# Optimization experiments

Measured on AMD Instinct MI355X. Metric: run time of the kernel, lower is better.

Reference implementation:

```python
import jax, jax.numpy as jnp
import numpy as np

B, I, H = 16384, 512, 512


def _linear_params(key, out_dim, in_dim):
    kw, kb = jax.random.split(key)
    bound = 1.0 / np.sqrt(in_dim)
    W = jax.random.uniform(kw, (out_dim, in_dim), jnp.float32, -bound, bound)
    b = jax.random.uniform(kb, (out_dim,), jnp.float32, -bound, bound)
    return W, b


def setup_inputs() -> dict:
    key = jax.random.key(0)
    ks = jax.random.split(key, 12)
    x = jax.random.normal(ks[0], (B, I), jnp.float32)
    h_prev = jax.random.normal(ks[1], (B, H), jnp.float32)
    c_prev = jax.random.normal(ks[2], (B, H), jnp.float32)
    W_xi, b_xi = _linear_params(ks[3], H, I)
    W_hi, b_hi = _linear_params(ks[4], H, H)
    W_xf, b_xf = _linear_params(ks[5], H, I)
    W_hf, b_hf = _linear_params(ks[6], H, H)
    W_xc, b_xc = _linear_params(ks[7], H, I)
    W_hc, b_hc = _linear_params(ks[8], H, H)
    W_xo, b_xo = _linear_params(ks[9], H, I)
    W_ho, b_ho = _linear_params(ks[10], H, H)
    W_e, b_e = _linear_params(ks[11], H, I + H)
    return dict(x=x, h_prev=h_prev, c_prev=c_prev,
                W_xi=W_xi, b_xi=b_xi, W_hi=W_hi, b_hi=b_hi,
                W_xf=W_xf, b_xf=b_xf, W_hf=W_hf, b_hf=b_hf,
                W_xc=W_xc, b_xc=b_xc, W_hc=W_hc, b_hc=b_hc,
                W_xo=W_xo, b_xo=b_xo, W_ho=W_ho, b_ho=b_ho,
                W_e=W_e, b_e=b_e)


def reference(x, h_prev, c_prev,
              W_xi, b_xi, W_hi, b_hi,
              W_xf, b_xf, W_hf, b_hf,
              W_xc, b_xc, W_hc, b_hc,
              W_xo, b_xo, W_ho, b_ho,
              W_e, b_e):
    # Batch the 4 input-to-hidden projections into one GEMM and the 4
    # hidden-to-hidden projections into another (same math as 8 Linears).
    Wx = jnp.concatenate([W_xi, W_xf, W_xc, W_xo], axis=0)   # [4H, I]
    bx = jnp.concatenate([b_xi, b_xf, b_xc, b_xo], axis=0)   # [4H]
    Wh = jnp.concatenate([W_hi, W_hf, W_hc, W_ho], axis=0)   # [4H, H]
    bh = jnp.concatenate([b_hi, b_hf, b_hc, b_ho], axis=0)
    gates = (x @ Wx.T + bx) + (h_prev @ Wh.T + bh)            # [B, 4H]
    gi, gf, gc, go = jnp.split(gates, 4, axis=-1)
    i = jax.nn.sigmoid(gi)
    f = jax.nn.sigmoid(gf)
    g = jnp.tanh(gc)
    o = jax.nn.sigmoid(go)
    c = f * c_prev + i * g
    # exp gate: Linear on [x, h_prev] -> tanh -> exp; split W_e to avoid concat
    We_x, We_h = W_e[:, :x.shape[-1]], W_e[:, x.shape[-1]:]
    exp_factor = jnp.exp(jnp.tanh(x @ We_x.T + h_prev @ We_h.T + b_e))
    h = o * jnp.tanh(c) * exp_factor
    return (h, c)
```

## Files before the change

### kernel.cpp

```cpp
#include <hip/hip_runtime.h>
#include <stdint.h>

#define Bsz 16384
#define Hh  512
#define Kd  1024
#define BM  256
#define BNJ 32
#define BK  64
#define NT  16

typedef __attribute__((ext_vector_type(8))) short bf16x8;
typedef __attribute__((ext_vector_type(4))) float f32x4;
typedef __attribute__((ext_vector_type(8))) unsigned short u16x8;

__device__ __forceinline__ unsigned short f2bf(float f) {
    union { float f; unsigned u; } v; v.f = f;
    unsigned u = v.u;
    return (unsigned short)((u + 0x7fffu + ((u >> 16) & 1u)) >> 16);
}
__device__ __forceinline__ float fast_tanh(float x) {
    float e = __expf(2.f * x);
    return (e - 1.f) / (e + 1.f);
}
__device__ __forceinline__ float fast_sigmoid(float x) {
    return 1.f / (1.f + __expf(-x));
}

__global__ void pack_A(const float* __restrict__ x, const float* __restrict__ h,
                       unsigned short* __restrict__ A) {
    const long total = (long)Bsz * Kd / 8;
    for (long i = (long)blockIdx.x * blockDim.x + threadIdx.x; i < total;
         i += (long)gridDim.x * blockDim.x) {
        long row = i >> 7;
        int  col = ((int)(i & 127)) << 3;
        const float* src = (col < 512) ? (x + row * 512 + col)
                                       : (h + row * 512 + (col - 512));
        float4 f0 = *(const float4*)(src);
        float4 f1 = *(const float4*)(src + 4);
        u16x8 o;
        o[0]=f2bf(f0.x); o[1]=f2bf(f0.y); o[2]=f2bf(f0.z); o[3]=f2bf(f0.w);
        o[4]=f2bf(f1.x); o[5]=f2bf(f1.y); o[6]=f2bf(f1.z); o[7]=f2bf(f1.w);
        *(u16x8*)(A + (i << 3)) = o;
    }
}

__global__ void pack_B(const float* __restrict__ Wxi, const float* __restrict__ Whi,
                       const float* __restrict__ Wxf, const float* __restrict__ Whf,
                       const float* __restrict__ Wxc, const float* __restrict__ Whc,
                       const float* __restrict__ Wxo, const float* __restrict__ Who,
                       const float* __restrict__ We,
                       const float* __restrict__ bxi, const float* __restrict__ bhi,
                       const float* __restrict__ bxf, const float* __restrict__ bhf,
                       const float* __restrict__ bxc, const float* __restrict__ bhc,
                       const float* __restrict__ bxo, const float* __restrict__ bho,
                       const float* __restrict__ be,
                       unsigned short* __restrict__ Bp, float* __restrict__ bias) {
    const long id = (long)blockIdx.x * blockDim.x + threadIdx.x;
    if (id < 327680) {
        int blk = (int)(id >> 6);
        int l   = (int)(id & 63);
        int kh  = blk & 1;
        int kt  = (blk >> 1) & 15;
        int rest = blk >> 5;
        int g    = rest % 5;
        int jgrp = rest / 5;
        int j  = jgrp * 16 + (l & 15);
        int k0 = kt * 64 + kh * 32 + ((l >> 4) << 3);
        const float* src;
        if (g == 4) {
            src = We + (long)j * 1024 + k0;
        } else {
            const float* Wx = (g == 0) ? Wxi : (g == 1) ? Wxf : (g == 2) ? Wxc : Wxo;
            const float* Wh = (g == 0) ? Whi : (g == 1) ? Whf : (g == 2) ? Whc : Who;
            src = (k0 < 512) ? (Wx + (long)j * 512 + k0)
                             : (Wh + (long)j * 512 + (k0 - 512));
        }
        float4 f0 = *(const float4*)(src);
        float4 f1 = *(const float4*)(src + 4);
        u16x8 o;
        o[0]=f2bf(f0.x); o[1]=f2bf(f0.y); o[2]=f2bf(f0.z); o[3]=f2bf(f0.w);
        o[4]=f2bf(f1.x); o[5]=f2bf(f1.y); o[6]=f2bf(f1.z); o[7]=f2bf(f1.w);
        *(u16x8*)(Bp + (long)blk * 512 + l * 8) = o;
    }
    if (id < 2560) {
        int row = (int)id;
        int g = row >> 9, j = row & 511;
        float b;
        if (g == 4) b = be[j];
        else {
            const float* bx = (g == 0) ? bxi : (g == 1) ? bxf : (g == 2) ? bxc : bxo;
            const float* bh = (g == 0) ? bhi : (g == 1) ? bhf : (g == 2) ? bhc : bho;
            b = bx[j] + bh[j];
        }
        bias[row] = b;
    }
}

#define GL16(g, l) __builtin_amdgcn_global_load_lds( \
    (const __attribute__((address_space(1))) unsigned int*)(g), \
    (__attribute__((address_space(3))) unsigned int*)(l), 16, 0, 0)

#define WAITVM(n) asm volatile("s_waitcnt vmcnt(" #n ")" ::: "memory")
#define WAITLGKM0() asm volatile("s_waitcnt lgkmcnt(0)" ::: "memory")
#define BARRIER() asm volatile("s_barrier" ::: "memory")

#define STAGE_A(BUF, T) do { \
    _Pragma("unroll") \
    for (int it_ = 0; it_ < 4; ++it_) { \
        int c_   = it_ * 512 + tid; \
        int row_ = c_ >> 3; \
        int ch_  = c_ & 7; \
        const unsigned short* src_ = A + (brow + row_) * (long)Kd + (T) * BK \
                                     + ((ch_ ^ (row_ & 7)) << 3); \
        GL16(src_, &Alds[BUF][c_ << 3]); \
    } \
} while (0)

#define LOADB(BN, T) do { \
    const unsigned short* bsrc_ = Bp + ((long)(jgrp * 160) + (T) * 2) * 512 + lane * 8; \
    _Pragma("unroll") \
    for (int g_ = 0; g_ < 5; ++g_) { \
        _Pragma("unroll") \
        for (int kh_ = 0; kh_ < 2; ++kh_) { \
            asm volatile("global_load_dwordx4 %0, %1, off" \
                : "=v"(BN[g_ * 2 + kh_]) \
                : "v"(bsrc_ + (g_ * 32 + kh_) * 512)); \
        } \
    } \
} while (0)

#define LOADA_FRAGS(BUF) do { \
    _Pragma("unroll") \
    for (int m_ = 0; m_ < 4; ++m_) { \
        int r_ = wm * 64 + m_ * 16 + fr; \
        _Pragma("unroll") \
        for (int kh_ = 0; kh_ < 2; ++kh_) { \
            af[m_][kh_] = *(const bf16x8*)&Alds[BUF][r_ * 64 + \
                ((((kh_ << 2) | q) ^ (fr & 7)) << 3)]; \
        } \
    } \
} while (0)

#define MFMA_CLUSTER(BC) do { \
    __builtin_amdgcn_s_setprio(1); \
    _Pragma("unroll") \
    for (int g_ = 0; g_ < 5; ++g_) \
        _Pragma("unroll") \
        for (int m_ = 0; m_ < 4; ++m_) \
            _Pragma("unroll") \
            for (int kh_ = 0; kh_ < 2; ++kh_) \
                acc[g_][m_] = __builtin_amdgcn_mfma_f32_16x16x32_bf16( \
                    af[m_][kh_], BC[g_ * 2 + kh_], acc[g_][m_], 0, 0, 0); \
    __builtin_amdgcn_s_setprio(0); \
} while (0)

#define ITER(T, BUF, BCUR, BNXT, WA, WB, IA, IB) do { \
    WAITVM(WA); \
    BARRIER(); \
    LOADA_FRAGS(BUF); \
    WAITLGKM0(); \
    BARRIER(); \
    if (IB) LOADB(BNXT, (T) + 1); \
    if (IA) STAGE_A(BUF, (T) + 2); \
    WAITVM(WB); \
    __builtin_amdgcn_sched_barrier(0); \
    MFMA_CLUSTER(BCUR); \
} while (0)

__global__ __launch_bounds__(512, 2)
void xlstm_gemm(const unsigned short* __restrict__ A,
                const unsigned short* __restrict__ Bp,
                const float* __restrict__ bias,
                const float* __restrict__ c_prev,
                float* __restrict__ out) {
    __shared__ __align__(16) unsigned short Alds[2][BM * BK];

    const int tid  = threadIdx.x;
    const int wid  = tid >> 6;
    const int lane = tid & 63;
    const int wm   = wid >> 1;
    const int wj   = wid & 1;
    const int fr   = lane & 15;
    const int q    = lane >> 4;

    const int orig = blockIdx.x;
    const int wg   = (orig & 7) * 128 + (orig >> 3);
    const int mblk = wg >> 4;
    const int jblk = wg & 15;
    const long brow = (long)mblk * BM;
    const int  bcol = jblk * BNJ;
    const int  jgrp = jblk * 2 + wj;

    f32x4 acc[5][4];
#pragma unroll
    for (int g = 0; g < 5; ++g)
#pragma unroll
        for (int m = 0; m < 4; ++m)
#pragma unroll
            for (int r = 0; r < 4; ++r) acc[g][m][r] = 0.f;

    bf16x8 af[4][2];
    bf16x8 BA[10], BB[10];

    STAGE_A(0, 0);
    LOADB(BA, 0);
    STAGE_A(1, 1);

    for (int t = 0; t < 14; t += 2) {
        ITER(t,     0, BA, BB, 14, 18, 1, 1);
        ITER(t + 1, 1, BB, BA, 14, 18, 1, 1);
    }
    ITER(14, 0, BA, BB, 14, 14, 0, 1);
    ITER(15, 1, BB, BA, 10,  0, 0, 0);

    const int j = bcol + wj * 16 + fr;
    const float bi_ = bias[j];
    const float bf_ = bias[512 + j];
    const float bc_ = bias[1024 + j];
    const float bo_ = bias[1536 + j];
    const float be_ = bias[2048 + j];
    const long mbase = brow + wm * 64 + (q << 2);
#pragma unroll
    for (int m = 0; m < 4; ++m) {
#pragma unroll
        for (int r = 0; r < 4; ++r) {
            long row = mbase + m * 16 + r;
            float gi = acc[0][m][r] + bi_;
            float gf = acc[1][m][r] + bf_;
            float gc = acc[2][m][r] + bc_;
            float go = acc[3][m][r] + bo_;
            float ge = acc[4][m][r] + be_;
            float iv = fast_sigmoid(gi);
            float fv = fast_sigmoid(gf);
            float gv = fast_tanh(gc);
            float ov = fast_sigmoid(go);
            float ef = __expf(fast_tanh(ge));
            float cp = c_prev[row * 512 + j];
            float cv = fv * cp + iv * gv;
            float hv = ov * fast_tanh(cv) * ef;
            out[row * 512 + j] = hv;
            out[(long)Bsz * 512 + row * 512 + j] = cv;
        }
    }
}

extern "C" void kernel_launch(void* const* d_in, const int* in_sizes, int n_in,
                              void* d_out, int out_size, void* d_ws, size_t ws_size,
                              hipStream_t stream) {
    const float* x      = (const float*)d_in[0];
    const float* h_prev = (const float*)d_in[1];
    const float* c_prev = (const float*)d_in[2];
    const float* Wxi = (const float*)d_in[3];
    const float* bxi = (const float*)d_in[4];
    const float* Whi = (const float*)d_in[5];
    const float* bhi = (const float*)d_in[6];
    const float* Wxf = (const float*)d_in[7];
    const float* bxf = (const float*)d_in[8];
    const float* Whf = (const float*)d_in[9];
    const float* bhf = (const float*)d_in[10];
    const float* Wxc = (const float*)d_in[11];
    const float* bxc = (const float*)d_in[12];
    const float* Whc = (const float*)d_in[13];
    const float* bhc = (const float*)d_in[14];
    const float* Wxo = (const float*)d_in[15];
    const float* bxo = (const float*)d_in[16];
    const float* Who = (const float*)d_in[17];
    const float* bho = (const float*)d_in[18];
    const float* We  = (const float*)d_in[19];
    const float* be  = (const float*)d_in[20];

    unsigned short* Abf  = (unsigned short*)d_ws;
    unsigned short* Bp   = (unsigned short*)((char*)d_ws + 33554432);
    float*          bias = (float*)((char*)d_ws + 33554432 + 5242880);

    pack_A<<<2048, 256, 0, stream>>>(x, h_prev, Abf);
    pack_B<<<1280, 256, 0, stream>>>(Wxi, Whi, Wxf, Whf, Wxc, Whc, Wxo, Who, We,
                                     bxi, bhi, bxf, bhf, bxc, bhc, bxo, bho, be,
                                     Bp, bias);
    xlstm_gemm<<<1024, 512, 0, stream>>>(Abf, Bp, bias, c_prev, (float*)d_out);
}
```

Measured before the change: 142.8 us.

## Deepen A-tile LDS pipeline to four buffers and interleave loads with MFMA phases

Replaces the two-stage loop with a four-buffer LDS ring for A, prefetching three tiles ahead. Each K-tile is split into four phases that each issue a slice of the next B register loads and one quarter of the A staging, interleaved with ten MFMAs. The aim is to hide global-load latency and spread memory issue across the compute. It doubles LDS use, which may limit occupancy, and adds barriers per phase with hand-tuned vmcnt waits that are fragile.

```diff
diff --git a/kernel.cpp b/kernel.cpp
--- a/kernel.cpp
+++ b/kernel.cpp
@@ -100,71 +100,56 @@
     (const __attribute__((address_space(1))) unsigned int*)(g), \
     (__attribute__((address_space(3))) unsigned int*)(l), 16, 0, 0)
 
-#define WAITVM(n) asm volatile("s_waitcnt vmcnt(" #n ")" ::: "memory")
+#define WAITVM_I(n) asm volatile("s_waitcnt vmcnt(" #n ")" ::: "memory")
+#define WAITVM(n) WAITVM_I(n)
 #define WAITLGKM0() asm volatile("s_waitcnt lgkmcnt(0)" ::: "memory")
 #define BARRIER() asm volatile("s_barrier" ::: "memory")
 
-#define STAGE_A(BUF, T) do { \
-    _Pragma("unroll") \
-    for (int it_ = 0; it_ < 4; ++it_) { \
-        int c_   = it_ * 512 + tid; \
-        int row_ = c_ >> 3; \
-        int ch_  = c_ & 7; \
-        const unsigned short* src_ = A + (brow + row_) * (long)Kd + (T) * BK \
-                                     + ((ch_ ^ (row_ & 7)) << 3); \
-        GL16(src_, &Alds[BUF][c_ << 3]); \
-    } \
+#define MF(a, b, c) __builtin_amdgcn_mfma_f32_16x16x32_bf16(a, b, c, 0, 0, 0)
+
+#define LB(BN, T, R) asm volatile("global_load_dwordx4 %0, %1, off" \
+    : "=v"(BN[R]) : "v"(bbase + (long)(T) * 1024 + ((R) >> 1) * 16384 + ((R) & 1) * 512))
+#define LBA(BN, T) do { LB(BN, T, 0); LB(BN, T, 2); LB(BN, T, 4); } while (0)
+#define LBB(BN, T) do { LB(BN, T, 6); LB(BN, T, 8); LB(BN, T, 1); } while (0)
+#define LBC(BN, T) do { LB(BN, T, 3); LB(BN, T, 5); } while (0)
+#define LBD(BN, T) do { LB(BN, T, 7); LB(BN, T, 9); } while (0)
+#define NOB() ((void)0)
+
+#define SGL(SB, T, P) GL16(A + srcoff + (P) * 65536 + (long)(T) * 64, \
+                           &Alds[SB][(P) * 4096 + tid * 8])
+#define SGL4(SB, T) do { SGL(SB,T,0); SGL(SB,T,1); SGL(SB,T,2); SGL(SB,T,3); } while (0)
+
+#define AF(RB, M, SWZ) (*(const bf16x8*)&Alds[RB][abase + (M) * 1024 + (SWZ)])
+
+#define PH(RB, BC, SWZ, KH, M0, M1, HW, WN, BI, SI) do { \
+    bf16x8 af0_ = AF(RB, M0, SWZ); \
+    bf16x8 af1_ = AF(RB, M1, SWZ); \
+    BI; \
+    SI; \
+    if (HW) WAITVM(WN); \
+    BARRIER(); \
+    WAITLGKM0(); \
+    __builtin_amdgcn_sched_barrier(0); \
+    __builtin_amdgcn_s_setprio(1); \
+    acc[0][M0] = MF(af0_, BC[0 + (KH)], acc[0][M0]); \
+    acc[0][M1] = MF(af1_, BC[0 + (KH)], acc[0][M1]); \
+    acc[1][M0] = MF(af0_, BC[2 + (KH)], acc[1][M0]); \
+    acc[1][M1] = MF(af1_, BC[2 + (KH)], acc[1][M1]); \
+    acc[2][M0] = MF(af0_, BC[4 + (KH)], acc[2][M0]); \
+    acc[2][M1] = MF(af1_, BC[4 + (KH)], acc[2][M1]); \
+    acc[3][M0] = MF(af0_, BC[6 + (KH)], acc[3][M0]); \
+    acc[3][M1] = MF(af1_, BC[6 + (KH)], acc[3][M1]); \
+    acc[4][M0] = MF(af0_, BC[8 + (KH)], acc[4][M0]); \
+    acc[4][M1] = MF(af1_, BC[8 + (KH)], acc[4][M1]); \
+    __builtin_amdgcn_s_setprio(0); \
+    BARRIER(); \
 } while (0)
 
-#define LOADB(BN, T) do { \
-    const unsigned short* bsrc_ = Bp + ((long)(jgrp * 160) + (T) * 2) * 512 + lane * 8; \
-    _Pragma("unroll") \
-    for (int g_ = 0; g_ < 5; ++g_) { \
-        _Pragma("unroll") \
-        for (int kh_ = 0; kh_ < 2; ++kh_) { \
-            asm volatile("global_load_dwordx4 %0, %1, off" \
-                : "=v"(BN[g_ * 2 + kh_]) \
-                : "v"(bsrc_ + (g_ * 32 + kh_) * 512)); \
-        } \
-    } \
-} while (0)
-
-#define LOADA_FRAGS(BUF) do { \
-    _Pragma("unroll") \
-    for (int m_ = 0; m_ < 4; ++m_) { \
-        int r_ = wm * 64 + m_ * 16 + fr; \
-        _Pragma("unroll") \
-        for (int kh_ = 0; kh_ < 2; ++kh_) { \
-            af[m_][kh_] = *(const bf16x8*)&Alds[BUF][r_ * 64 + \
-                ((((kh_ << 2) | q) ^ (fr & 7)) << 3)]; \
-        } \
-    } \
-} while (0)
-
-#define MFMA_CLUSTER(BC) do { \
-    __builtin_amdgcn_s_setprio(1); \
-    _Pragma("unroll") \
-    for (int g_ = 0; g_ < 5; ++g_) \
-        _Pragma("unroll") \
-        for (int m_ = 0; m_ < 4; ++m_) \
-            _Pragma("unroll") \
-            for (int kh_ = 0; kh_ < 2; ++kh_) \
-                acc[g_][m_] = __builtin_amdgcn_mfma_f32_16x16x32_bf16( \
-                    af[m_][kh_], BC[g_ * 2 + kh_], acc[g_][m_], 0, 0, 0); \
-    __builtin_amdgcn_s_setprio(0); \
-} while (0)
-
-#define ITER(T, BUF, BCUR, BNXT, WA, WB, IA, IB) do { \
-    WAITVM(WA); \
-    BARRIER(); \
-    LOADA_FRAGS(BUF); \
-    WAITLGKM0(); \
-    BARRIER(); \
-    if (IB) LOADB(BNXT, (T) + 1); \
-    if (IA) STAGE_A(BUF, (T) + 2); \
-    WAITVM(WB); \
-    __builtin_amdgcn_sched_barrier(0); \
-    MFMA_CLUSTER(BCUR); \
+#define TILE_FULL(TN, RB, SB, BC, BN) do { \
+    PH(RB, BC, swz0, 0, 0, 1, 1, 10, LBA(BN, (TN) + 1), SGL(SB, (TN) + 3, 0)); \
+    PH(RB, BC, swz0, 0, 2, 3, 0, 0,  LBB(BN, (TN) + 1), SGL(SB, (TN) + 3, 1)); \
+    PH(RB, BC, swz1, 1, 0, 1, 1, 11, LBC(BN, (TN) + 1), SGL(SB, (TN) + 3, 2)); \
+    PH(RB, BC, swz1, 1, 2, 3, 1, 28, LBD(BN, (TN) + 1), SGL(SB, (TN) + 3, 3)); \
 } while (0)
 
 __global__ __launch_bounds__(512, 2)
@@ -173,7 +158,7 @@
                 const float* __restrict__ bias,
                 const float* __restrict__ c_prev,
                 float* __restrict__ out) {
-    __shared__ __align__(16) unsigned short Alds[2][BM * BK];
+    __shared__ __align__(16) unsigned short Alds[4][BM * BK];
 
     const int tid  = threadIdx.x;
     const int wid  = tid >> 6;
@@ -199,19 +184,40 @@
 #pragma unroll
             for (int r = 0; r < 4; ++r) acc[g][m][r] = 0.f;
 
-    bf16x8 af[4][2];
     bf16x8 BA[10], BB[10];
 
-    STAGE_A(0, 0);
-    LOADB(BA, 0);
-    STAGE_A(1, 1);
-
-    for (int t = 0; t < 14; t += 2) {
-        ITER(t,     0, BA, BB, 14, 18, 1, 1);
-        ITER(t + 1, 1, BB, BA, 14, 18, 1, 1);
-    }
-    ITER(14, 0, BA, BB, 14, 14, 0, 1);
-    ITER(15, 1, BB, BA, 10,  0, 0, 0);
+    const int r0_ = tid >> 3;
+    const long srcoff = (brow + r0_) * 1024L + (((tid & 7) ^ (r0_ & 7)) << 3);
+    const unsigned short* bbase = Bp + (long)jgrp * 81920 + lane * 8;
+    const int abase = (wm * 64 + fr) * 64;
+    const int swz0 = ((q) ^ (fr & 7)) << 3;
+    const int swz1 = ((4 | q) ^ (fr & 7)) << 3;
+
+    SGL4(0, 0); SGL4(1, 1); SGL4(2, 2);
+    LBA(BA, 0); LBB(BA, 0); LBC(BA, 0); LBD(BA, 0);
+    WAITVM(0);
+    BARRIER();
+
+    for (int tq = 0; tq < 12; tq += 4) {
+        TILE_FULL(tq + 0, 0, 3, BA, BB);
+        TILE_FULL(tq + 1, 1, 0, BB, BA);
+        TILE_FULL(tq + 2, 2, 1, BA, BB);
+        TILE_FULL(tq + 3, 3, 2, BB, BA);
+    }
+    TILE_FULL(12, 0, 3, BA, BB);
+
+    PH(1, BB, swz0, 0, 0, 1, 1, 9,  LBA(BA, 14), NOB());
+    PH(1, BB, swz0, 0, 2, 3, 0, 0,  LBB(BA, 14), NOB());
+    PH(1, BB, swz1, 1, 0, 1, 1, 8,  LBC(BA, 14), NOB());
+    PH(1, BB, swz1, 1, 2, 3, 1, 24, LBD(BA, 14), NOB());
+    PH(2, BA, swz0, 0, 0, 1, 1, 7,  LBA(BB, 15), NOB());
+    PH(2, BA, swz0, 0, 2, 3, 0, 0,  LBB(BB, 15), NOB());
+    PH(2, BA, swz1, 1, 0, 1, 1, 8,  LBC(BB, 15), NOB());
+    PH(2, BA, swz1, 1, 2, 3, 1, 20, LBD(BB, 15), NOB());
+    PH(3, BB, swz0, 0, 0, 1, 1, 4,  NOB(), NOB());
+    PH(3, BB, swz0, 0, 2, 3, 0, 0,  NOB(), NOB());
+    PH(3, BB, swz1, 1, 0, 1, 1, 0,  NOB(), NOB());
+    PH(3, BB, swz1, 1, 2, 3, 0, 0,  NOB(), NOB());
 
     const int j = bcol + wj * 16 + fr;
     const float bi_ = bias[j];
```

After: 143.1 us. About the same (+0.2%).

## Stage B tiles through LDS with triple-buffered interleaved loads

Applied to the files above, without the earlier changes.

B fragments now go through LDS with direct global-to-LDS loads alongside A, instead of being loaded straight into registers. A three-buffer ring replaces the double buffer, and each K tile is split into four MFMA sub-clusters with staging loads interleaved between them. This frees the 20 B vector registers and spreads memory issue across the compute phases. In exchange it adds LDS reads and more barriers, and the larger shared-memory footprint may limit occupancy.

```diff
diff --git a/kernel.cpp b/kernel.cpp
--- a/kernel.cpp
+++ b/kernel.cpp
@@ -8,6 +8,8 @@
 #define BNJ 32
 #define BK  64
 #define NT  16
+
+#define BUFB 53248
 
 typedef __attribute__((ext_vector_type(8))) short bf16x8;
 typedef __attribute__((ext_vector_type(4))) float f32x4;
@@ -100,71 +102,93 @@
     (const __attribute__((address_space(1))) unsigned int*)(g), \
     (__attribute__((address_space(3))) unsigned int*)(l), 16, 0, 0)
 
-#define WAITVM(n) asm volatile("s_waitcnt vmcnt(" #n ")" ::: "memory")
+#define WAITVM_I(n) asm volatile("s_waitcnt vmcnt(" #n ")" ::: "memory")
+#define WAITVM(n) WAITVM_I(n)
 #define WAITLGKM0() asm volatile("s_waitcnt lgkmcnt(0)" ::: "memory")
 #define BARRIER() asm volatile("s_barrier" ::: "memory")
-
-#define STAGE_A(BUF, T) do { \
-    _Pragma("unroll") \
-    for (int it_ = 0; it_ < 4; ++it_) { \
-        int c_   = it_ * 512 + tid; \
-        int row_ = c_ >> 3; \
-        int ch_  = c_ & 7; \
-        const unsigned short* src_ = A + (brow + row_) * (long)Kd + (T) * BK \
-                                     + ((ch_ ^ (row_ & 7)) << 3); \
-        GL16(src_, &Alds[BUF][c_ << 3]); \
+#define SCHED0() __builtin_amdgcn_sched_barrier(0)
+
+#define MF(a, b, c) __builtin_amdgcn_mfma_f32_16x16x32_bf16(a, b, c, 0, 0, 0)
+
+#define SGT(SBUF, TT, I) GL16(sb##I + (long)(TT) * sstr##I, \
+    lds_raw + (SBUF) * BUFB + sld##I)
+
+#define LOADB5(BUF, KH) do { \
+    b0 = *(const bf16x8*)(lds_raw + (BUF)*BUFB + bbyte + 0*2048 + (KH)*1024); \
+    b1 = *(const bf16x8*)(lds_raw + (BUF)*BUFB + bbyte + 1*2048 + (KH)*1024); \
+    b2 = *(const bf16x8*)(lds_raw + (BUF)*BUFB + bbyte + 2*2048 + (KH)*1024); \
+    b3 = *(const bf16x8*)(lds_raw + (BUF)*BUFB + bbyte + 3*2048 + (KH)*1024); \
+    b4 = *(const bf16x8*)(lds_raw + (BUF)*BUFB + bbyte + 4*2048 + (KH)*1024); \
+} while (0)
+
+#define LOADA2(BUF, M0, M1, SWZ) do { \
+    af0 = *(const bf16x8*)(lds_raw + (BUF)*BUFB + abyte + (M0)*2048 + (SWZ)); \
+    af1 = *(const bf16x8*)(lds_raw + (BUF)*BUFB + abyte + (M1)*2048 + (SWZ)); \
+} while (0)
+
+#define MFMA10(M0, M1) do { \
+    __builtin_amdgcn_s_setprio(1); \
+    acc[0][M0] = MF(af0, b0, acc[0][M0]); acc[0][M1] = MF(af1, b0, acc[0][M1]); \
+    acc[1][M0] = MF(af0, b1, acc[1][M0]); acc[1][M1] = MF(af1, b1, acc[1][M1]); \
+    acc[2][M0] = MF(af0, b2, acc[2][M0]); acc[2][M1] = MF(af1, b2, acc[2][M1]); \
+    acc[3][M0] = MF(af0, b3, acc[3][M0]); acc[3][M1] = MF(af1, b3, acc[3][M1]); \
+    acc[4][M0] = MF(af0, b4, acc[4][M0]); acc[4][M1] = MF(af1, b4, acc[4][M1]); \
+    __builtin_amdgcn_s_setprio(0); \
+} while (0)
+
+#define TILE_STD(T, BUF, SBUF) do { \
+    LOADB5(BUF, 0); LOADA2(BUF, 0, 1, swz0); \
+    SGT(SBUF, (T)+2, 0); SGT(SBUF, (T)+2, 1); \
+    BARRIER(); WAITLGKM0(); SCHED0(); MFMA10(0, 1); BARRIER(); \
+    LOADA2(BUF, 2, 3, swz0); \
+    SGT(SBUF, (T)+2, 2); SGT(SBUF, (T)+2, 3); \
+    BARRIER(); WAITLGKM0(); SCHED0(); MFMA10(2, 3); BARRIER(); \
+    LOADB5(BUF, 1); LOADA2(BUF, 0, 1, swz1); \
+    SGT(SBUF, (T)+2, 4); SGT(SBUF, (T)+2, 5); \
+    BARRIER(); WAITLGKM0(); SCHED0(); MFMA10(0, 1); BARRIER(); \
+    LOADA2(BUF, 2, 3, swz1); \
+    SGT(SBUF, (T)+2, 6); \
+    WAITVM(7); \
+    BARRIER(); WAITLGKM0(); SCHED0(); MFMA10(2, 3); BARRIER(); \
+} while (0)
+
+#define TILE_T14(BUF) do { \
+    LOADB5(BUF, 0); LOADA2(BUF, 0, 1, swz0); \
+    BARRIER(); WAITLGKM0(); SCHED0(); MFMA10(0, 1); BARRIER(); \
+    LOADA2(BUF, 2, 3, swz0); \
+    BARRIER(); WAITLGKM0(); SCHED0(); MFMA10(2, 3); BARRIER(); \
+    LOADB5(BUF, 1); LOADA2(BUF, 0, 1, swz1); \
+    BARRIER(); WAITLGKM0(); SCHED0(); MFMA10(0, 1); BARRIER(); \
+    LOADA2(BUF, 2, 3, swz1); \
+    WAITVM(0); \
+    BARRIER(); WAITLGKM0(); SCHED0(); MFMA10(2, 3); BARRIER(); \
+} while (0)
+
+#define TILE_T15(BUF) do { \
+    LOADB5(BUF, 0); LOADA2(BUF, 0, 1, swz0); \
+    BARRIER(); WAITLGKM0(); SCHED0(); MFMA10(0, 1); BARRIER(); \
+    LOADA2(BUF, 2, 3, swz0); \
+    BARRIER(); WAITLGKM0(); SCHED0(); MFMA10(2, 3); BARRIER(); \
+    LOADB5(BUF, 1); LOADA2(BUF, 0, 1, swz1); \
+    BARRIER(); WAITLGKM0(); SCHED0(); MFMA10(0, 1); BARRIER(); \
+    LOADA2(BUF, 2, 3, swz1); \
+    BARRIER(); WAITLGKM0(); SCHED0(); MFMA10(2, 3); \
+} while (0)
+
+#define INIT_SLOT(I) do { \
+    int c_ = wid * 7 + (I); if (c_ >= 52) c_ -= 52; \
+    if (c_ < 32) { \
+        sb##I   = A + (brow + 8 * c_ + (lane >> 3)) * 1024L \
+                    + (((lane & 7) ^ ((lane >> 3) & 7)) << 3); \
+        sstr##I = 64; \
+        sld##I  = c_ * 1024; \
+    } else { \
+        int b_ = c_ - 32; int jl_ = b_ / 10; int rem_ = b_ - jl_ * 10; \
+        sb##I   = Bp + (long)(jblk * 2 + jl_) * 81920 \
+                    + (rem_ >> 1) * 16384 + (rem_ & 1) * 512 + lane * 8; \
+        sstr##I = 1024; \
+        sld##I  = 32768 + b_ * 1024; \
     } \
-} while (0)
-
-#define LOADB(BN, T) do { \
-    const unsigned short* bsrc_ = Bp + ((long)(jgrp * 160) + (T) * 2) * 512 + lane * 8; \
-    _Pragma("unroll") \
-    for (int g_ = 0; g_ < 5; ++g_) { \
-        _Pragma("unroll") \
-        for (int kh_ = 0; kh_ < 2; ++kh_) { \
-            asm volatile("global_load_dwordx4 %0, %1, off" \
-                : "=v"(BN[g_ * 2 + kh_]) \
-                : "v"(bsrc_ + (g_ * 32 + kh_) * 512)); \
-        } \
-    } \
-} while (0)
-
-#define LOADA_FRAGS(BUF) do { \
-    _Pragma("unroll") \
-    for (int m_ = 0; m_ < 4; ++m_) { \
-        int r_ = wm * 64 + m_ * 16 + fr; \
-        _Pragma("unroll") \
-        for (int kh_ = 0; kh_ < 2; ++kh_) { \
-            af[m_][kh_] = *(const bf16x8*)&Alds[BUF][r_ * 64 + \
-                ((((kh_ << 2) | q) ^ (fr & 7)) << 3)]; \
-        } \
-    } \
-} while (0)
-
-#define MFMA_CLUSTER(BC) do { \
-    __builtin_amdgcn_s_setprio(1); \
-    _Pragma("unroll") \
-    for (int g_ = 0; g_ < 5; ++g_) \
-        _Pragma("unroll") \
-        for (int m_ = 0; m_ < 4; ++m_) \
-            _Pragma("unroll") \
-            for (int kh_ = 0; kh_ < 2; ++kh_) \
-                acc[g_][m_] = __builtin_amdgcn_mfma_f32_16x16x32_bf16( \
-                    af[m_][kh_], BC[g_ * 2 + kh_], acc[g_][m_], 0, 0, 0); \
-    __builtin_amdgcn_s_setprio(0); \
-} while (0)
-
-#define ITER(T, BUF, BCUR, BNXT, WA, WB, IA, IB) do { \
-    WAITVM(WA); \
-    BARRIER(); \
-    LOADA_FRAGS(BUF); \
-    WAITLGKM0(); \
-    BARRIER(); \
-    if (IB) LOADB(BNXT, (T) + 1); \
-    if (IA) STAGE_A(BUF, (T) + 2); \
-    WAITVM(WB); \
-    __builtin_amdgcn_sched_barrier(0); \
-    MFMA_CLUSTER(BCUR); \
 } while (0)
 
 __global__ __launch_bounds__(512, 2)
@@ -173,7 +197,7 @@
                 const float* __restrict__ bias,
                 const float* __restrict__ c_prev,
                 float* __restrict__ out) {
-    __shared__ __align__(16) unsigned short Alds[2][BM * BK];
+    __shared__ __align__(16) unsigned char lds_raw[3 * BUFB];
 
     const int tid  = threadIdx.x;
     const int wid  = tid >> 6;
@@ -189,7 +213,6 @@
     const int jblk = wg & 15;
     const long brow = (long)mblk * BM;
     const int  bcol = jblk * BNJ;
-    const int  jgrp = jblk * 2 + wj;
 
     f32x4 acc[5][4];
 #pragma unroll
@@ -199,19 +222,35 @@
 #pragma unroll
             for (int r = 0; r < 4; ++r) acc[g][m][r] = 0.f;
 
-    bf16x8 af[4][2];
-    bf16x8 BA[10], BB[10];
-
-    STAGE_A(0, 0);
-    LOADB(BA, 0);
-    STAGE_A(1, 1);
-
-    for (int t = 0; t < 14; t += 2) {
-        ITER(t,     0, BA, BB, 14, 18, 1, 1);
-        ITER(t + 1, 1, BB, BA, 14, 18, 1, 1);
-    }
-    ITER(14, 0, BA, BB, 14, 14, 0, 1);
-    ITER(15, 1, BB, BA, 10,  0, 0, 0);
+    bf16x8 af0, af1, b0, b1, b2, b3, b4;
+
+    const int abyte = (wm * 64 + fr) * 128;
+    const int bbyte = 32768 + wj * 10240 + lane * 16;
+    const int swz0  = ((q) ^ (fr & 7)) << 4;
+    const int swz1  = ((4 | q) ^ (fr & 7)) << 4;
+
+    const unsigned short *sb0, *sb1, *sb2, *sb3, *sb4, *sb5, *sb6;
+    int sstr0, sstr1, sstr2, sstr3, sstr4, sstr5, sstr6;
+    int sld0, sld1, sld2, sld3, sld4, sld5, sld6;
+    INIT_SLOT(0); INIT_SLOT(1); INIT_SLOT(2); INIT_SLOT(3);
+    INIT_SLOT(4); INIT_SLOT(5); INIT_SLOT(6);
+
+    SGT(0, 0, 0); SGT(0, 0, 1); SGT(0, 0, 2); SGT(0, 0, 3);
+    SGT(0, 0, 4); SGT(0, 0, 5); SGT(0, 0, 6);
+    SGT(1, 1, 0); SGT(1, 1, 1); SGT(1, 1, 2); SGT(1, 1, 3);
+    SGT(1, 1, 4); SGT(1, 1, 5); SGT(1, 1, 6);
+    WAITVM(7);
+    BARRIER();
+
+    for (int t = 0; t < 12; t += 3) {
+        TILE_STD(t,     0, 2);
+        TILE_STD(t + 1, 1, 0);
+        TILE_STD(t + 2, 2, 1);
+    }
+    TILE_STD(12, 0, 2);
+    TILE_STD(13, 1, 0);
+    TILE_T14(2);
+    TILE_T15(0);
 
     const int j = bcol + wj * 16 + fr;
     const float bi_ = bias[j];
```

New measurement: 129.2 us. -9.5%, faster.

## Double N tile and stage B through LDS with interleaved MFMA pipeline

Applied to the files above, without the earlier changes.

Widens the per-block output tile from 32 to 64 hidden columns across all five gates, halving the grid. The B weight fragments are now staged into LDS with global_load_lds instead of being loaded directly into registers. Each wave reads A and B fragments from LDS, overlapping those reads with MFMA clusters using fine-grained lgkmcnt waits. Per-block LDS use rises to about 144KB, and the accumulator count doubles. This reduces how often A is re-read per output column, but may reduce occupancy to one block per CU and add register pressure.

```diff
diff --git a/kernel.cpp b/kernel.cpp
--- a/kernel.cpp
+++ b/kernel.cpp
@@ -5,9 +5,11 @@
 #define Hh  512
 #define Kd  1024
 #define BM  256
-#define BNJ 32
+#define BNJ 64
 #define BK  64
 #define NT  16
+
+#define LDSB 73728
 
 typedef __attribute__((ext_vector_type(8))) short bf16x8;
 typedef __attribute__((ext_vector_type(4))) float f32x4;
@@ -100,71 +102,72 @@
     (const __attribute__((address_space(1))) unsigned int*)(g), \
     (__attribute__((address_space(3))) unsigned int*)(l), 16, 0, 0)
 
-#define WAITVM(n) asm volatile("s_waitcnt vmcnt(" #n ")" ::: "memory")
-#define WAITLGKM0() asm volatile("s_waitcnt lgkmcnt(0)" ::: "memory")
-#define BARRIER() asm volatile("s_barrier" ::: "memory")
-
-#define STAGE_A(BUF, T) do { \
-    _Pragma("unroll") \
-    for (int it_ = 0; it_ < 4; ++it_) { \
-        int c_   = it_ * 512 + tid; \
-        int row_ = c_ >> 3; \
-        int ch_  = c_ & 7; \
-        const unsigned short* src_ = A + (brow + row_) * (long)Kd + (T) * BK \
-                                     + ((ch_ ^ (row_ & 7)) << 3); \
-        GL16(src_, &Alds[BUF][c_ << 3]); \
-    } \
-} while (0)
-
-#define LOADB(BN, T) do { \
-    const unsigned short* bsrc_ = Bp + ((long)(jgrp * 160) + (T) * 2) * 512 + lane * 8; \
+#define WAITVM0()  asm volatile("s_waitcnt vmcnt(0)" ::: "memory")
+#define LGKM_I(n)  asm volatile("s_waitcnt lgkmcnt(" #n ")" ::: "memory")
+#define LGKM(n)    LGKM_I(n)
+#define BARRIER()  asm volatile("s_barrier" ::: "memory")
+#define SCHED0()   __builtin_amdgcn_sched_barrier(0)
+
+#define MF(a, b, c) __builtin_amdgcn_mfma_f32_16x16x32_bf16(a, b, c, 0, 0, 0)
+
+#define RDA(KH, APTR) do { \
+    afA[KH][0] = *(const bf16x8*)((APTR) + 0 * 2048); \
+    afA[KH][1] = *(const bf16x8*)((APTR) + 1 * 2048); \
+    afA[KH][2] = *(const bf16x8*)((APTR) + 2 * 2048); \
+    afA[KH][3] = *(const bf16x8*)((APTR) + 3 * 2048); \
+} while (0)
+
+#define RDB(SET, BPTR, JF, KH) do { \
+    SET[0] = *(const bf16x8*)((BPTR) + ((JF)*10 + 0 + (KH)) * 1024); \
+    SET[1] = *(const bf16x8*)((BPTR) + ((JF)*10 + 2 + (KH)) * 1024); \
+    SET[2] = *(const bf16x8*)((BPTR) + ((JF)*10 + 4 + (KH)) * 1024); \
+    SET[3] = *(const bf16x8*)((BPTR) + ((JF)*10 + 6 + (KH)) * 1024); \
+    SET[4] = *(const bf16x8*)((BPTR) + ((JF)*10 + 8 + (KH)) * 1024); \
+} while (0)
+
+#define SGA(SO, T) do { \
+    GL16(asrc + 0 * 65536 + (T) * 64, lds_raw + (SO) + adst + 0 * 8192); \
+    GL16(asrc + 1 * 65536 + (T) * 64, lds_raw + (SO) + adst + 1 * 8192); \
+    GL16(asrc + 2 * 65536 + (T) * 64, lds_raw + (SO) + adst + 2 * 8192); \
+    GL16(asrc + 3 * 65536 + (T) * 64, lds_raw + (SO) + adst + 3 * 8192); \
+} while (0)
+
+#define SGB(SO, T) do { \
+    GL16(bstg0 + (T) * 1024, lds_raw + (SO) + bdst + 0 * 1024); \
+    GL16(bstg1 + (T) * 1024, lds_raw + (SO) + bdst + 1 * 1024); \
+    GL16(bstg2 + (T) * 1024, lds_raw + (SO) + bdst + 2 * 1024); \
+    GL16(bstg3 + (T) * 1024, lds_raw + (SO) + bdst + 3 * 1024); \
+    GL16(bstg4 + (T) * 1024, lds_raw + (SO) + bdst + 4 * 1024); \
+} while (0)
+
+#define MFMA20(KH, JF, BSET) do { \
+    __builtin_amdgcn_s_setprio(1); \
     _Pragma("unroll") \
     for (int g_ = 0; g_ < 5; ++g_) { \
-        _Pragma("unroll") \
-        for (int kh_ = 0; kh_ < 2; ++kh_) { \
-            asm volatile("global_load_dwordx4 %0, %1, off" \
-                : "=v"(BN[g_ * 2 + kh_]) \
-                : "v"(bsrc_ + (g_ * 32 + kh_) * 512)); \
-        } \
+        acc[g_][0][JF] = MF(afA[KH][0], BSET[g_], acc[g_][0][JF]); \
+        acc[g_][1][JF] = MF(afA[KH][1], BSET[g_], acc[g_][1][JF]); \
+        acc[g_][2][JF] = MF(afA[KH][2], BSET[g_], acc[g_][2][JF]); \
+        acc[g_][3][JF] = MF(afA[KH][3], BSET[g_], acc[g_][3][JF]); \
     } \
-} while (0)
-
-#define LOADA_FRAGS(BUF) do { \
-    _Pragma("unroll") \
-    for (int m_ = 0; m_ < 4; ++m_) { \
-        int r_ = wm * 64 + m_ * 16 + fr; \
-        _Pragma("unroll") \
-        for (int kh_ = 0; kh_ < 2; ++kh_) { \
-            af[m_][kh_] = *(const bf16x8*)&Alds[BUF][r_ * 64 + \
-                ((((kh_ << 2) | q) ^ (fr & 7)) << 3)]; \
-        } \
-    } \
-} while (0)
-
-#define MFMA_CLUSTER(BC) do { \
-    __builtin_amdgcn_s_setprio(1); \
-    _Pragma("unroll") \
-    for (int g_ = 0; g_ < 5; ++g_) \
-        _Pragma("unroll") \
-        for (int m_ = 0; m_ < 4; ++m_) \
-            _Pragma("unroll") \
-            for (int kh_ = 0; kh_ < 2; ++kh_) \
-                acc[g_][m_] = __builtin_amdgcn_mfma_f32_16x16x32_bf16( \
-                    af[m_][kh_], BC[g_ * 2 + kh_], acc[g_][m_], 0, 0, 0); \
     __builtin_amdgcn_s_setprio(0); \
 } while (0)
 
-#define ITER(T, BUF, BCUR, BNXT, WA, WB, IA, IB) do { \
-    WAITVM(WA); \
-    BARRIER(); \
-    LOADA_FRAGS(BUF); \
-    WAITLGKM0(); \
-    BARRIER(); \
-    if (IB) LOADB(BNXT, (T) + 1); \
-    if (IA) STAGE_A(BUF, (T) + 2); \
-    WAITVM(WB); \
-    __builtin_amdgcn_sched_barrier(0); \
-    MFMA_CLUSTER(BCUR); \
+#define TILE(APK0, APK1, BPTR, SO, T, STG, SYNC) do { \
+    RDA(0, APK0); RDB(bs0, BPTR, 0, 0); SCHED0(); \
+    RDB(bs1, BPTR, 1, 0); SCHED0(); \
+    if (STG) { SGB(SO, (T) + 1); } SCHED0(); \
+    LGKM(5); SCHED0(); \
+    MFMA20(0, 0, bs0); SCHED0(); \
+    RDA(1, APK1); RDB(bs0, BPTR, 0, 1); SCHED0(); \
+    if (STG) { SGA(SO, (T) + 1); } SCHED0(); \
+    LGKM(9); SCHED0(); \
+    MFMA20(0, 1, bs1); SCHED0(); \
+    RDB(bs1, BPTR, 1, 1); SCHED0(); \
+    LGKM(5); SCHED0(); \
+    MFMA20(1, 0, bs0); SCHED0(); \
+    LGKM(0); SCHED0(); \
+    MFMA20(1, 1, bs1); SCHED0(); \
+    if (SYNC) { WAITVM0(); BARRIER(); } \
 } while (0)
 
 __global__ __launch_bounds__(512, 2)
@@ -173,7 +176,7 @@
                 const float* __restrict__ bias,
                 const float* __restrict__ c_prev,
                 float* __restrict__ out) {
-    __shared__ __align__(16) unsigned short Alds[2][BM * BK];
+    __shared__ __align__(16) unsigned char lds_raw[2 * LDSB];
 
     const int tid  = threadIdx.x;
     const int wid  = tid >> 6;
@@ -184,62 +187,89 @@
     const int q    = lane >> 4;
 
     const int orig = blockIdx.x;
-    const int wg   = (orig & 7) * 128 + (orig >> 3);
-    const int mblk = wg >> 4;
-    const int jblk = wg & 15;
+    const int wg   = (orig & 7) * 64 + (orig >> 3);
+    const int mblk = wg >> 3;
+    const int jblk = wg & 7;
     const long brow = (long)mblk * BM;
     const int  bcol = jblk * BNJ;
-    const int  jgrp = jblk * 2 + wj;
-
-    f32x4 acc[5][4];
+
+    f32x4 acc[5][4][2];
 #pragma unroll
     for (int g = 0; g < 5; ++g)
 #pragma unroll
         for (int m = 0; m < 4; ++m)
 #pragma unroll
-            for (int r = 0; r < 4; ++r) acc[g][m][r] = 0.f;
-
-    bf16x8 af[4][2];
-    bf16x8 BA[10], BB[10];
-
-    STAGE_A(0, 0);
-    LOADB(BA, 0);
-    STAGE_A(1, 1);
+            for (int jf = 0; jf < 2; ++jf)
+#pragma unroll
+                for (int r = 0; r < 4; ++r) acc[g][m][jf][r] = 0.f;
+
+    bf16x8 afA[2][4];
+    bf16x8 bs0[5], bs1[5];
+
+    const int aboff = (wm * 64 + fr) * 128;
+    const int swz0  = ((q) ^ (fr & 7)) << 4;
+    const int swz1  = ((4 | q) ^ (fr & 7)) << 4;
+    const unsigned char* aP0k0 = lds_raw + aboff + swz0;
+    const unsigned char* aP0k1 = lds_raw + aboff + swz1;
+    const unsigned char* aP1k0 = aP0k0 + LDSB;
+    const unsigned char* aP1k1 = aP0k1 + LDSB;
+    const unsigned char* bP0 = lds_raw + 32768 + wj * 20480 + lane * 16;
+    const unsigned char* bP1 = bP0 + LDSB;
+
+    const int r0_ = tid >> 3;
+    const unsigned short* asrc = A + (brow + r0_) * 1024L
+                                   + (((tid & 7) ^ (r0_ & 7)) << 3);
+    const int adst = tid * 16;
+    const int bdst = 32768 + wid * 5120 + lane * 16;
+    const int c0_ = wid * 5;
+    const unsigned short* bstg0 = Bp + (long)(jblk*4 + (c0_+0)/10)*81920 + (((c0_+0)%10)>>1)*16384 + ((c0_+0)&1)*512 + lane*8;
+    const unsigned short* bstg1 = Bp + (long)(jblk*4 + (c0_+1)/10)*81920 + (((c0_+1)%10)>>1)*16384 + ((c0_+1)&1)*512 + lane*8;
+    const unsigned short* bstg2 = Bp + (long)(jblk*4 + (c0_+2)/10)*81920 + (((c0_+2)%10)>>1)*16384 + ((c0_+2)&1)*512 + lane*8;
+    const unsigned short* bstg3 = Bp + (long)(jblk*4 + (c0_+3)/10)*81920 + (((c0_+3)%10)>>1)*16384 + ((c0_+3)&1)*512 + lane*8;
+    const unsigned short* bstg4 = Bp + (long)(jblk*4 + (c0_+4)/10)*81920 + (((c0_+4)%10)>>1)*16384 + ((c0_+4)&1)*512 + lane*8;
+
+    SGB(0, 0);
+    SGA(0, 0);
+    WAITVM0();
+    BARRIER();
 
     for (int t = 0; t < 14; t += 2) {
-        ITER(t,     0, BA, BB, 14, 18, 1, 1);
-        ITER(t + 1, 1, BB, BA, 14, 18, 1, 1);
-    }
-    ITER(14, 0, BA, BB, 14, 14, 0, 1);
-    ITER(15, 1, BB, BA, 10,  0, 0, 0);
-
-    const int j = bcol + wj * 16 + fr;
-    const float bi_ = bias[j];
-    const float bf_ = bias[512 + j];
-    const float bc_ = bias[1024 + j];
-    const float bo_ = bias[1536 + j];
-    const float be_ = bias[2048 + j];
+        TILE(aP0k0, aP0k1, bP0, LDSB, t,     1, 1);
+        TILE(aP1k0, aP1k1, bP1, 0,    t + 1, 1, 1);
+    }
+    TILE(aP0k0, aP0k1, bP0, LDSB, 14, 1, 1);
+    TILE(aP1k0, aP1k1, bP1, 0,    15, 0, 0);
+
     const long mbase = brow + wm * 64 + (q << 2);
 #pragma unroll
-    for (int m = 0; m < 4; ++m) {
-#pragma unroll
-        for (int r = 0; r < 4; ++r) {
-            long row = mbase + m * 16 + r;
-            float gi = acc[0][m][r] + bi_;
-            float gf = acc[1][m][r] + bf_;
-            float gc = acc[2][m][r] + bc_;
-            float go = acc[3][m][r] + bo_;
-            float ge = acc[4][m][r] + be_;
-            float iv = fast_sigmoid(gi);
-            float fv = fast_sigmoid(gf);
-            float gv = fast_tanh(gc);
-            float ov = fast_sigmoid(go);
-            float ef = __expf(fast_tanh(ge));
-            float cp = c_prev[row * 512 + j];
-            float cv = fv * cp + iv * gv;
-            float hv = ov * fast_tanh(cv) * ef;
-            out[row * 512 + j] = hv;
-            out[(long)Bsz * 512 + row * 512 + j] = cv;
+    for (int jf = 0; jf < 2; ++jf) {
+        const int j = bcol + wj * 32 + jf * 16 + fr;
+        const float bi_ = bias[j];
+        const float bf_ = bias[512 + j];
+        const float bc_ = bias[1024 + j];
+        const float bo_ = bias[1536 + j];
+        const float be_ = bias[2048 + j];
+#pragma unroll
+        for (int m = 0; m < 4; ++m) {
+#pragma unroll
+            for (int r = 0; r < 4; ++r) {
+                long row = mbase + m * 16 + r;
+                float gi = acc[0][m][jf][r] + bi_;
+                float gf = acc[1][m][jf][r] + bf_;
+                float gc = acc[2][m][jf][r] + bc_;
+                float go = acc[3][m][jf][r] + bo_;
+                float ge = acc[4][m][jf][r] + be_;
+                float iv = fast_sigmoid(gi);
+                float fv = fast_sigmoid(gf);
+                float gv = fast_tanh(gc);
+                float ov = fast_sigmoid(go);
+                float ef = __expf(fast_tanh(ge));
+                float cp = c_prev[row * 512 + j];
+                float cv = fv * cp + iv * gv;
+                float hv = ov * fast_tanh(cv) * ef;
+                out[row * 512 + j] = hv;
+                out[(long)Bsz * 512 + row * 512 + j] = cv;
+            }
         }
     }
 }
@@ -277,5 +307,5 @@
     pack_B<<<1280, 256, 0, stream>>>(Wxi, Whi, Wxf, Whf, Wxc, Whc, Wxo, Who, We,
                                      bxi, bhi, bxf, bhf, bxc, bhc, bxo, bho, be,
                                      Bp, bias);
-    xlstm_gemm<<<1024, 512, 0, stream>>>(Abf, Bp, bias, c_prev, (float*)d_out);
-}
+    xlstm_gemm<<<512, 512, 0, stream>>>(Abf, Bp, bias, c_prev, (float*)d_out);
+}
```

Result: slower. 197.8 us (+38.6%).
